# Kernel optimization log

Hardware: AMD Instinct MI355X
Metric: run time of the kernel (lower is better)

## Reference

```python
import jax, jax.numpy as jnp
import numpy as np

B, T, C = 2, 2048, 768
H, N_LEFT = 12, 6
D = C // H


def setup_inputs() -> dict:
    key = jax.random.key(0)
    ks = jax.random.split(key, 4)
    x = jax.random.normal(ks[0], (B, T, C), dtype=jnp.float32)
    attention_mask = jnp.ones((B, T), dtype=jnp.int32)
    Wqkv_w = jax.random.normal(ks[1], (3 * C, C), dtype=jnp.float32) * (C ** -0.5)
    Wqkv_b = jnp.zeros((3 * C,), dtype=jnp.float32)
    Wo_w = jax.random.normal(ks[2], (C, C), dtype=jnp.float32) * (C ** -0.5)
    Wo_b = jnp.zeros((C,), dtype=jnp.float32)
    return {"x": x, "attention_mask": attention_mask, "Wqkv_w": Wqkv_w,
            "Wqkv_b": Wqkv_b, "Wo_w": Wo_w, "Wo_b": Wo_b}


def _attend(q, k, v, mask):
    # q,k,v: [B,h,T,D]; mask: [B,1,T,T] additive
    s = jnp.einsum('bhqd,bhkd->bhqk', q, k) * (D ** -0.5) + mask
    a = jax.nn.softmax(s.astype(jnp.float32), axis=-1).astype(q.dtype)
    return jnp.einsum('bhqk,bhkd->bhqd', a, v)


def reference(x, attention_mask, Wqkv_w, Wqkv_b, Wo_w, Wo_b):
    neg = jnp.finfo(x.dtype).min
    # padding mask [B,1,1,T]: 0 where valid, neg where padded
    pad = (1.0 - attention_mask.astype(x.dtype))[:, None, None, :] * neg
    i = jnp.arange(T)
    tri = (i[None, :] > i[:, None]).astype(x.dtype) * neg   # triu(neg, 1)
    left_mask = tri[None, None] + pad                        # causal (look left)
    right_mask = tri.T[None, None] + pad                     # anti-causal (look right)

    qkv = (x @ Wqkv_w.T + Wqkv_b).reshape(B, T, 3, H, D)
    qkv = jnp.transpose(qkv, (0, 3, 2, 1, 4))                # [B,H,3,T,D]
    q, k, v = qkv[:, :, 0], qkv[:, :, 1], qkv[:, :, 2]

    lc = _attend(q[:, :N_LEFT], k[:, :N_LEFT], v[:, :N_LEFT], left_mask)
    rc = _attend(q[:, N_LEFT:], k[:, N_LEFT:], v[:, N_LEFT:], right_mask)
    ctx = jnp.concatenate([lc, rc], axis=1)                  # [B,H,T,D]
    ctx = jnp.transpose(ctx, (0, 2, 1, 3)).reshape(B, T, C)
    out = ctx @ Wo_w.T + Wo_b
    return out
```

## Files before the change

kernel.cpp:

```cpp
#include <hip/hip_runtime.h>


typedef unsigned short u16;
typedef __bf16 bf16x8 __attribute__((ext_vector_type(8)));
typedef float fx4 __attribute__((ext_vector_type(4)));
typedef unsigned short u16x8 __attribute__((ext_vector_type(8)));
typedef unsigned short u16x4 __attribute__((ext_vector_type(4)));
typedef _Float16 hx4 __attribute__((ext_vector_type(4)));
typedef __fp16 fp16x2 __attribute__((ext_vector_type(2)));

#define T_SEQ 2048
#define C_DIM 768
#define NHEAD 12
#define HDIM  64
#define NITEMS 768
#define LOG2E_8 0.18033688f

__device__ __forceinline__ u16 f2bf(float f) {
  unsigned u = __float_as_uint(f);
  u += 0x7fffu + ((u >> 16) & 1u);
  return (u16)(u >> 16);
}
__device__ __forceinline__ u16 f2h(float f) {
  union { _Float16 h; u16 u; } cv; cv.h = (_Float16)f; return cv.u;
}

__device__ __forceinline__ void gl2lds16(const u16* g, u16* l) {
  __builtin_amdgcn_global_load_lds(
      (const __attribute__((address_space(1))) void*)g,
      (__attribute__((address_space(3))) void*)l, 16, 0, 0);
}

__global__ void cvt_all_k(const float* __restrict__ x,
                          const float* __restrict__ wqkv,
                          const float* __restrict__ wo,
                          const int* __restrict__ am,
                          u16* __restrict__ out, float* __restrict__ mf,
                          unsigned* __restrict__ fbits, int* __restrict__ cnt) {
  if (blockIdx.x >= 2688) {
    int bid = blockIdx.x - 2688;
    int i = bid * blockDim.x + threadIdx.x;
    if (i < 4096) mf[i] = am[i] ? 0.f : -1e30f;
    if (bid == 16) {
      int t = threadIdx.x;
      if (t == 0) cnt[0] = 0;
      if (t < 64) {
        int bb = t >> 5, kt = t & 31;
        const int* seg = am + (bb << 11) + (kt << 6);
        int anyz = 0;
        for (int j = 0; j < 64; ++j) anyz |= (seg[j] == 0);
        unsigned long long bal = __ballot(anyz != 0);
        if (t == 0)  fbits[0] = (unsigned)(bal & 0xffffffffull);
        if (t == 32) fbits[1] = (unsigned)(bal >> 32);
      }
    }
    return;
  }
  int i = blockIdx.x * blockDim.x + threadIdx.x;
  int m = i / 96;
  int c8 = (i - m * 96) << 3;
  const float* src;
  if (m < 4096)       src = x    + (size_t)m * C_DIM + c8;
  else if (m < 6400)  src = wqkv + (size_t)(m - 4096) * C_DIM + c8;
  else                src = wo   + (size_t)(m - 6400) * C_DIM + c8;
  fx4 a = *(const fx4*)src, b = *(const fx4*)(src + 4);
  u16x8 o;
  #pragma unroll
  for (int j = 0; j < 4; ++j) { o[j] = f2bf(a[j]); o[4 + j] = f2bf(b[j]); }
  *(u16x8*)&out[(size_t)m * C_DIM + (c8 ^ ((m & 7) << 3))] = o;
}

__device__ __forceinline__ void gemm_core_64x128(const u16* __restrict__ A,
                                                 const u16* __restrict__ B,
                                                 int m0, int n0,
                                                 u16* As, u16* Bs,
                                                 fx4 acc[4][2]) {
  const int tid = threadIdx.x;
  const int lane = tid & 63, wv = tid >> 6;
  const int wn = wv << 5;
  const int lr = lane & 15, lg = lane >> 4;
  const int swk = (lr & 7) << 3;
  const int scol = (tid & 7) << 3;
  #pragma unroll
  for (int mt = 0; mt < 4; ++mt)
    #pragma unroll
    for (int nt = 0; nt < 2; ++nt) acc[mt][nt] = fx4{0.f, 0.f, 0.f, 0.f};

  #pragma unroll
  for (int p = 0; p < 2; ++p) {
    int row = (tid >> 3) + (p << 5);
    gl2lds16(&A[(size_t)(m0 + row) * C_DIM + scol], &As[(row << 6) + scol]);
  }
  #pragma unroll
  for (int p = 0; p < 4; ++p) {
    int row = (tid >> 3) + (p << 5);
    gl2lds16(&B[(size_t)(n0 + row) * C_DIM + scol], &Bs[(row << 6) + scol]);
  }

  int buf = 0;
  for (int k0 = 0; k0 < C_DIM; k0 += 64, buf ^= 1) {
    __syncthreads();
    if (k0 + 64 < C_DIM) {
      u16* Ad = &As[(buf ^ 1) << 12];
      u16* Bd = &Bs[(buf ^ 1) << 13];
      #pragma unroll
      for (int p = 0; p < 2; ++p) {
        int row = (tid >> 3) + (p << 5);
        gl2lds16(&A[(size_t)(m0 + row) * C_DIM + k0 + 64 + scol], &Ad[(row << 6) + scol]);
      }
      #pragma unroll
      for (int p = 0; p < 4; ++p) {
        int row = (tid >> 3) + (p << 5);
        gl2lds16(&B[(size_t)(n0 + row) * C_DIM + k0 + 64 + scol], &Bd[(row << 6) + scol]);
      }
    }
    const u16* Ab = &As[buf << 12];
    const u16* Bb = &Bs[buf << 13];
    #pragma unroll
    for (int kk = 0; kk < 64; kk += 32) {
      bf16x8 af[4], bfr[2];
      #pragma unroll
      for (int mt = 0; mt < 4; ++mt)
        af[mt] = *(const bf16x8*)&Ab[((mt * 16 + lr) << 6) + ((kk + lg * 8) ^ swk)];
      #pragma unroll
      for (int nt = 0; nt < 2; ++nt)
        bfr[nt] = *(const bf16x8*)&Bb[((wn + nt * 16 + lr) << 6) + ((kk + lg * 8) ^ swk)];
      #pragma unroll
      for (int mt = 0; mt < 4; ++mt)
        #pragma unroll
        for (int nt = 0; nt < 2; ++nt)
          acc[mt][nt] = __builtin_amdgcn_mfma_f32_16x16x32_bf16(
              af[mt], bfr[nt], acc[mt][nt], 0, 0, 0);
    }
  }
}

__global__ __launch_bounds__(256) void gemm_qkv_k(
    const u16* __restrict__ A, const u16* __restrict__ B,
    const float* __restrict__ bias,
    u16* __restrict__ qb, u16* __restrict__ kswz, u16* __restrict__ vswz) {
  __shared__ __align__(16) u16 As[2][64 * 64];
  __shared__ __align__(16) u16 Bs[2][128 * 64];
  int m0 = blockIdx.y << 6, n0 = blockIdx.x << 7;
  fx4 acc[4][2];
  gemm_core_64x128(A, B, m0, n0, &As[0][0], &Bs[0][0], acc);

  const int tid = threadIdx.x, lane = tid & 63, wv = tid >> 6;
  const int wn = wv << 5;
  const int lr = lane & 15, lg = lane >> 4;
  const int part = n0 / 768;
  const int n0r = n0 - part * 768;
  const int bb = m0 >> 11, kt = (m0 >> 6) & 31;
  u16* Sc = &Bs[0][0];
  __syncthreads();

  if (part < 2) {
    #pragma unroll
    for (int nt = 0; nt < 2; ++nt) {
      int nl = wn + nt * 16 + lr;
      float bv = bias[n0 + nl];
      #pragma unroll
      for (int mt = 0; mt < 4; ++mt) {
        #pragma unroll
        for (int r = 0; r < 4; ++r) {
          int m = mt * 16 + lg * 4 + r;
          Sc[(m << 7) + (nl ^ ((m & 15) << 2))] = f2bf(acc[mt][nt][r] + bv);
        }
      }
    }
    __syncthreads();
    int c4 = (tid & 31) << 2;
    int ng = n0r + c4;
    int h = ng >> 6, d = ng & 63;
    int bh = bb * NHEAD + h;
    #pragma unroll
    for (int p = 0; p < 8; ++p) {
      int m = (tid >> 5) + (p << 3);
      u16x4 v = *(const u16x4*)&Sc[(m << 7) + (c4 ^ ((m & 15) << 2))];
      if (part == 0) {
        int t = (m0 & 2047) + m;
        *(u16x4*)&qb[(((size_t)bh << 11) + t) * HDIM + d] = v;
      } else {
        *(u16x4*)&kswz[((size_t)(bh * 32 + kt) << 12) + (m << 6) +
                       (d ^ ((m & 7) << 3))] = v;
      }
    }
  } else {
    #pragma unroll
    for (int nt = 0; nt < 2; ++nt) {
      int nl = wn + nt * 16 + lr;
      float bv = bias[n0 + nl];
      #pragma unroll
      for (int mt = 0; mt < 4; ++mt) {
        u16x4 pk;
        #pragma unroll
        for (int r = 0; r < 4; ++r) pk[r] = f2h(acc[mt][nt][r] + bv);
        int m4 = (mt << 2) + lg;
        *(u16x4*)&Sc[(nl << 6) + ((m4 ^ (nl & 15)) << 2)] = pk;
      }
    }
    __syncthreads();
    int tr4 = tid & 15;
    #pragma unroll
    for (int p = 0; p < 8; ++p) {
      int nl = (tid >> 4) + (p << 4);
      int ng = n0r + nl;
      int h = ng >> 6, d = ng & 63;
      u16x4 v = *(const u16x4*)&Sc[(nl << 6) + ((tr4 ^ (nl & 15)) << 2)];
      size_t tile = (size_t)((bb * NHEAD + h) * 32 + kt) << 12;
      *(u16x4*)&vswz[tile + (d << 6) + ((tr4 ^ (d & 15)) << 2)] = v;
    }
  }
}

__device__ __forceinline__ void gemm_core_64x64(const u16* __restrict__ A,
                                                const u16* __restrict__ B,
                                                int m0, int n0,
                                                u16* As, u16* Bs,
                                                fx4 acc[2][2]) {
  const int tid = threadIdx.x;
  const int lane = tid & 63, wv = tid >> 6;
  const int wm = (wv & 1) << 5, wn = (wv >> 1) << 5;
  const int lr = lane & 15, lg = lane >> 4;
  const int swk = (lr & 7) << 3;
  const int scol = (tid & 7) << 3;
  #pragma unroll
  for (int mt = 0; mt < 2; ++mt)
    #pragma unroll
    for (int nt = 0; nt < 2; ++nt) acc[mt][nt] = fx4{0.f, 0.f, 0.f, 0.f};

  #pragma unroll
  for (int p = 0; p < 2; ++p) {
    int row = (tid >> 3) + (p << 5);
    gl2lds16(&A[(size_t)(m0 + row) * C_DIM + scol], &As[(row << 6) + scol]);
    gl2lds16(&B[(size_t)(n0 + row) * C_DIM + scol], &Bs[(row << 6) + scol]);
  }

  int buf = 0;
  for (int k0 = 0; k0 < C_DIM; k0 += 64, buf ^= 1) {
    __syncthreads();
    if (k0 + 64 < C_DIM) {
      u16* Ad = &As[(buf ^ 1) << 12];
      u16* Bd = &Bs[(buf ^ 1) << 12];
      #pragma unroll
      for (int p = 0; p < 2; ++p) {
        int row = (tid >> 3) + (p << 5);
        gl2lds16(&A[(size_t)(m0 + row) * C_DIM + k0 + 64 + scol], &Ad[(row << 6) + scol]);
        gl2lds16(&B[(size_t)(n0 + row) * C_DIM + k0 + 64 + scol], &Bd[(row << 6) + scol]);
      }
    }
    const u16* Ab = &As[buf << 12];
    const u16* Bb = &Bs[buf << 12];
    #pragma unroll
    for (int kk = 0; kk < 64; kk += 32) {
      bf16x8 af[2], bfr[2];
      #pragma unroll
      for (int mt = 0; mt < 2; ++mt)
        af[mt] = *(const bf16x8*)&Ab[((wm + mt * 16 + lr) << 6) + ((kk + lg * 8) ^ swk)];
      #pragma unroll
      for (int nt = 0; nt < 2; ++nt)
        bfr[nt] = *(const bf16x8*)&Bb[((wn + nt * 16 + lr) << 6) + ((kk + lg * 8) ^ swk)];
      #pragma unroll
      for (int mt = 0; mt < 2; ++mt)
        #pragma unroll
        for (int nt = 0; nt < 2; ++nt)
          acc[mt][nt] = __builtin_amdgcn_mfma_f32_16x16x32_bf16(
              af[mt], bfr[nt], acc[mt][nt], 0, 0, 0);
    }
  }
}

__global__ __launch_bounds__(256) void gemm_out_k(
    const u16* __restrict__ A, const u16* __restrict__ B,
    const float* __restrict__ bias, float* __restrict__ out) {
  __shared__ __align__(16) u16 As[2][64 * 64];
  __shared__ __align__(16) u16 Bs[2][64 * 64];
  int m0 = blockIdx.y << 6, n0 = blockIdx.x << 6;
  fx4 acc[2][2];
  gemm_core_64x64(A, B, m0, n0, &As[0][0], &Bs[0][0], acc);

  const int tid = threadIdx.x, lane = tid & 63, wv = tid >> 6;
  const int wm = (wv & 1) << 5, wn = (wv >> 1) << 5;
  const int lr = lane & 15, lg = lane >> 4;
  #pragma unroll
  for (int nt = 0; nt < 2; ++nt) {
    int n = n0 + wn + nt * 16 + lr;
    float bv = bias[n];
    #pragma unroll
    for (int mt = 0; mt < 2; ++mt) {
      #pragma unroll
      for (int r = 0; r < 4; ++r) {
        int m = m0 + wm + mt * 16 + lg * 4 + r;
        out[(size_t)m * C_DIM + n] = acc[mt][nt][r] + bv;
      }
    }
  }
}

__global__ __launch_bounds__(256) void attn_k(
    const u16* __restrict__ q, const u16* __restrict__ kswz,
    const u16* __restrict__ vswz, const float* __restrict__ maskf,
    const unsigned* __restrict__ fbits,
    u16* __restrict__ ctx, int* __restrict__ counter) {
  __shared__ __align__(16) u16 Ks[2][4096];
  __shared__ __align__(16) u16 Vt[2][4096];
  __shared__ int s_w;

  const int tid = threadIdx.x, lane = tid & 63, wv = tid >> 6;
  const int lr = lane & 15, lg = lane >> 4;
  const int swk = (lr & 7) << 3;
  const int swv = (lr & 15) << 2;

  for (;;) {
    if (tid == 0) s_w = atomicAdd(counter, 1);
    __syncthreads();
    int w = s_w;
    if (w >= NITEMS) break;
    int qslot = w / 24, bh = w - qslot * 24;
    int bb = bh / NHEAD, h = bh - bb * NHEAD;
    bool causal = (h < 6);
    int qt = causal ? (31 - qslot) : qslot;
    int kt0 = causal ? 0 : qt;
    int kt1 = causal ? qt : 31;
    size_t tile_base = (size_t)(bh * 32) << 12;
    unsigned fb = fbits[bb];

    {
      const u16* kg = kswz + tile_base + ((size_t)kt0 << 12);
      const u16* vg = vswz + tile_base + ((size_t)kt0 << 12);
      #pragma unroll
      for (int c2 = 0; c2 < 2; ++c2) {
        int e = (wv << 10) + (c2 << 9) + (lane << 3);
        gl2lds16(kg + e, &Ks[0][e]);
        gl2lds16(vg + e, &Vt[0][e]);
      }
    }

    int q0 = qt << 6;
    size_t head_off = ((size_t)bh << 11) * HDIM;
    int qrow = q0 + wv * 16 + lr;
    bf16x8 qf0 = *(const bf16x8*)&q[head_off + (size_t)qrow * HDIM + lg * 8];
    bf16x8 qf1 = *(const bf16x8*)&q[head_off + (size_t)qrow * HDIM + 32 + lg * 8];
    const float* mrow = maskf + (bb << 11);

    fx4 o[4];
    #pragma unroll
    for (int dt = 0; dt < 4; ++dt) o[dt] = fx4{0.f, 0.f, 0.f, 0.f};
    float l_i = 0.f;

    int buf = 0;
    for (int kt = kt0; kt <= kt1; ++kt, buf ^= 1) {
      __syncthreads();
      if (kt < kt1) {
        const u16* kg = kswz + tile_base + ((size_t)(kt + 1) << 12);
        const u16* vg = vswz + tile_base + ((size_t)(kt + 1) << 12);
        #pragma unroll
        for (int c2 = 0; c2 < 2; ++c2) {
          int e = (wv << 10) + (c2 << 9) + (lane << 3);
          gl2lds16(kg + e, &Ks[buf ^ 1][e]);
          gl2lds16(vg + e, &Vt[buf ^ 1][e]);
        }
      }

      fx4 st[4];
      #pragma unroll
      for (int nt = 0; nt < 4; ++nt) {
        const u16* kr = &Ks[buf][(nt * 16 + lr) << 6];
        bf16x8 kf0 = *(const bf16x8*)&kr[(lg * 8) ^ swk];
        bf16x8 kf1 = *(const bf16x8*)&kr[(32 + lg * 8) ^ swk];
        fx4 z = fx4{0.f, 0.f, 0.f, 0.f};
        z = __builtin_amdgcn_mfma_f32_16x16x32_bf16(kf0, qf0, z, 0, 0, 0);
        st[nt] = __builtin_amdgcn_mfma_f32_16x16x32_bf16(kf1, qf1, z, 0, 0, 0);
      }

      float psum = 0.f;
      if (kt == qt) {
        #pragma unroll
        for (int nt = 0; nt < 4; ++nt) {
          int kb0 = (kt << 6) + nt * 16 + lg * 4;
          fx4 mv = *(const fx4*)&mrow[kb0];
          #pragma unroll
          for (int r = 0; r < 4; ++r) {
            float arg = st[nt][r] * LOG2E_8 + mv[r];
            int kabs = kb0 + r;
            bool dead = causal ? (kabs > qrow) : (kabs < qrow);
            arg = dead ? -1e30f : arg;
            float p = __builtin_amdgcn_exp2f(arg);
            st[nt][r] = p;
            psum += p;
          }
        }
      } else if ((fb >> kt) & 1u) {
        #pragma unroll
        for (int nt = 0; nt < 4; ++nt) {
          int kb0 = (kt << 6) + nt * 16 + lg * 4;
          fx4 mv = *(const fx4*)&mrow[kb0];
          #pragma unroll
          for (int r = 0; r < 4; ++r) {
            float p = __builtin_amdgcn_exp2f(st[nt][r] * LOG2E_8 + mv[r]);
            st[nt][r] = p;
            psum += p;
          }
        }
      } else {
        #pragma unroll
        for (int nt = 0; nt < 4; ++nt)
          #pragma unroll
          for (int r = 0; r < 4; ++r) {
            float p = __builtin_amdgcn_exp2f(st[nt][r] * LOG2E_8);
            st[nt][r] = p;
            psum += p;
          }
      }
      l_i += psum;

      #pragma unroll
      for (int nt = 0; nt < 4; ++nt) {
        union { hx4 v; fp16x2 hh[2]; } pu;
        pu.hh[0] = __builtin_amdgcn_cvt_pkrtz(st[nt][0], st[nt][1]);
        pu.hh[1] = __builtin_amdgcn_cvt_pkrtz(st[nt][2], st[nt][3]);
        hx4 pf = pu.v;
        #pragma unroll
        for (int dt = 0; dt < 4; ++dt) {
          const u16* vr = &Vt[buf][(dt * 16 + lr) << 6];
          hx4 vf = *(const hx4*)&vr[(nt * 16 + lg * 4) ^ swv];
          o[dt] = __builtin_amdgcn_mfma_f32_16x16x16f16(vf, pf, o[dt], 0, 0, 0);
        }
      }
    }

    l_i += __shfl_xor(l_i, 16, 64);
    l_i += __shfl_xor(l_i, 32, 64);
    float inv = 1.f / l_i;
    size_t rowb = ((size_t)(bb << 11) + qrow) * C_DIM;
    int csw = (qrow & 7) << 3;
    #pragma unroll
    for (int dt = 0; dt < 4; ++dt) {
      u16x4 pk;
      #pragma unroll
      for (int r = 0; r < 4; ++r) pk[r] = f2bf(o[dt][r] * inv);
      int colb = h * HDIM + dt * 16 + lg * 4;
      *(u16x4*)&ctx[rowb + (colb ^ csw)] = pk;
    }
  }
}

extern "C" void kernel_launch(void* const* d_in, const int* in_sizes, int n_in,
                              void* d_out, int out_size, void* d_ws, size_t ws_size,
                              hipStream_t stream) {
  const float* x     = (const float*)d_in[0];
  const int*   amask = (const int*)d_in[1];
  const float* wqkv  = (const float*)d_in[2];
  const float* bqkv  = (const float*)d_in[3];
  const float* wo    = (const float*)d_in[4];
  const float* bo    = (const float*)d_in[5];
  float* out = (float*)d_out;

  char* ws = (char*)d_ws;
  u16*      xb    = (u16*)(ws + 0);
  u16*      wqkvb = (u16*)(ws + 6291456);
  u16*      wob   = (u16*)(ws + 9830400);
  u16*      qb    = (u16*)(ws + 11010048);
  u16*      kswz  = (u16*)(ws + 17301504);
  u16*      vswz  = (u16*)(ws + 23592960);
  u16*      ctxb  = (u16*)(ws + 29884416);
  float*    maskf = (float*)(ws + 36175872);
  int*      cnt   = (int*)(ws + 36192256);
  unsigned* fbits = (unsigned*)(ws + 36192320);

  cvt_all_k<<<2705, 256, 0, stream>>>(x, wqkv, wo, amask, xb,
                                      maskf, fbits, cnt);

  gemm_qkv_k<<<dim3(18, 64), 256, 0, stream>>>(xb, wqkvb, bqkv, qb, kswz, vswz);
  attn_k<<<512, 256, 0, stream>>>(qb, kswz, vswz, maskf, fbits, ctxb, cnt);
  gemm_out_k<<<dim3(12, 64), 256, 0, stream>>>(ctxb, wob, bo, out);
}
```

Baseline: 165.7 us.

## Split key tile across waves instead of query rows, reduce partial outputs in LDS

Each wave now takes a 16-key slice of the 64-key tile for all 64 query rows, rather than 16 query rows against all 64 keys. K and V fragments are loaded once per tile per wave and reused across four query groups, which cuts LDS reads, while Q stays in registers as 4x2 fragments. The cost is a cross-wave reduction at the end: partial O accumulators and row sums are combined through LDS with extra barriers. Register pressure also rises because each wave now holds sixteen O accumulators. Softmax keeps using no max subtraction, so the partial sums can simply be added.

Result: faster. 162.4 us (median of 2 runs) (-2.0%).

```diff
diff --git a/kernel.cpp b/kernel.cpp
--- a/kernel.cpp
+++ b/kernel.cpp
@@ -304,12 +304,19 @@
     u16* __restrict__ ctx, int* __restrict__ counter) {
   __shared__ __align__(16) u16 Ks[2][4096];
   __shared__ __align__(16) u16 Vt[2][4096];
+  __shared__ float Ls[4][64];
   __shared__ int s_w;
 
   const int tid = threadIdx.x, lane = tid & 63, wv = tid >> 6;
   const int lr = lane & 15, lg = lane >> 4;
   const int swk = (lr & 7) << 3;
   const int swv = (lr & 15) << 2;
+  const int ke0 = ((wv * 16 + lr) << 6) + ((lg * 8) ^ swk);
+  const int ke1 = ((wv * 16 + lr) << 6) + (((32 + lg * 8)) ^ swk);
+  int vek[4];
+  #pragma unroll
+  for (int dt = 0; dt < 4; ++dt)
+    vek[dt] = ((dt * 16 + lr) << 6) + ((wv * 16 + lg * 4) ^ swv);
 
   for (;;) {
     if (tid == 0) s_w = atomicAdd(counter, 1);
@@ -338,15 +345,21 @@
 
     int q0 = qt << 6;
     size_t head_off = ((size_t)bh << 11) * HDIM;
-    int qrow = q0 + wv * 16 + lr;
-    bf16x8 qf0 = *(const bf16x8*)&q[head_off + (size_t)qrow * HDIM + lg * 8];
-    bf16x8 qf1 = *(const bf16x8*)&q[head_off + (size_t)qrow * HDIM + 32 + lg * 8];
+    bf16x8 qf[4][2];
+    #pragma unroll
+    for (int g = 0; g < 4; ++g) {
+      int qr = q0 + g * 16 + lr;
+      qf[g][0] = *(const bf16x8*)&q[head_off + (size_t)qr * HDIM + lg * 8];
+      qf[g][1] = *(const bf16x8*)&q[head_off + (size_t)qr * HDIM + 32 + lg * 8];
+    }
     const float* mrow = maskf + (bb << 11);
 
-    fx4 o[4];
-    #pragma unroll
-    for (int dt = 0; dt < 4; ++dt) o[dt] = fx4{0.f, 0.f, 0.f, 0.f};
-    float l_i = 0.f;
+    fx4 o[4][4];
+    #pragma unroll
+    for (int dt = 0; dt < 4; ++dt)
+      #pragma unroll
+      for (int g = 0; g < 4; ++g) o[dt][g] = fx4{0.f, 0.f, 0.f, 0.f};
+    float l[4] = {0.f, 0.f, 0.f, 0.f};
 
     int buf = 0;
     for (int kt = kt0; kt <= kt1; ++kt, buf ^= 1) {
@@ -362,85 +375,128 @@
         }
       }
 
+      const u16* kb = &Ks[buf][0];
+      const u16* vbl = &Vt[buf][0];
+
+      bf16x8 kf0 = *(const bf16x8*)&kb[ke0];
+      bf16x8 kf1 = *(const bf16x8*)&kb[ke1];
       fx4 st[4];
       #pragma unroll
-      for (int nt = 0; nt < 4; ++nt) {
-        const u16* kr = &Ks[buf][(nt * 16 + lr) << 6];
-        bf16x8 kf0 = *(const bf16x8*)&kr[(lg * 8) ^ swk];
-        bf16x8 kf1 = *(const bf16x8*)&kr[(32 + lg * 8) ^ swk];
+      for (int g = 0; g < 4; ++g) {
         fx4 z = fx4{0.f, 0.f, 0.f, 0.f};
-        z = __builtin_amdgcn_mfma_f32_16x16x32_bf16(kf0, qf0, z, 0, 0, 0);
-        st[nt] = __builtin_amdgcn_mfma_f32_16x16x32_bf16(kf1, qf1, z, 0, 0, 0);
-      }
-
-      float psum = 0.f;
+        z = __builtin_amdgcn_mfma_f32_16x16x32_bf16(kf0, qf[g][0], z, 0, 0, 0);
+        st[g] = __builtin_amdgcn_mfma_f32_16x16x32_bf16(kf1, qf[g][1], z, 0, 0, 0);
+      }
+
+      int kb0 = (kt << 6) + wv * 16 + lg * 4;
       if (kt == qt) {
-        #pragma unroll
-        for (int nt = 0; nt < 4; ++nt) {
-          int kb0 = (kt << 6) + nt * 16 + lg * 4;
-          fx4 mv = *(const fx4*)&mrow[kb0];
+        fx4 mv = *(const fx4*)&mrow[kb0];
+        #pragma unroll
+        for (int g = 0; g < 4; ++g) {
+          int qr = q0 + g * 16 + lr;
           #pragma unroll
           for (int r = 0; r < 4; ++r) {
-            float arg = st[nt][r] * LOG2E_8 + mv[r];
+            float arg = st[g][r] * LOG2E_8 + mv[r];
             int kabs = kb0 + r;
-            bool dead = causal ? (kabs > qrow) : (kabs < qrow);
+            bool dead = causal ? (kabs > qr) : (kabs < qr);
             arg = dead ? -1e30f : arg;
             float p = __builtin_amdgcn_exp2f(arg);
-            st[nt][r] = p;
-            psum += p;
+            st[g][r] = p;
+            l[g] += p;
           }
         }
       } else if ((fb >> kt) & 1u) {
-        #pragma unroll
-        for (int nt = 0; nt < 4; ++nt) {
-          int kb0 = (kt << 6) + nt * 16 + lg * 4;
-          fx4 mv = *(const fx4*)&mrow[kb0];
+        fx4 mv = *(const fx4*)&mrow[kb0];
+        #pragma unroll
+        for (int g = 0; g < 4; ++g)
           #pragma unroll
           for (int r = 0; r < 4; ++r) {
-            float p = __builtin_amdgcn_exp2f(st[nt][r] * LOG2E_8 + mv[r]);
-            st[nt][r] = p;
-            psum += p;
+            float p = __builtin_amdgcn_exp2f(st[g][r] * LOG2E_8 + mv[r]);
+            st[g][r] = p;
+            l[g] += p;
           }
-        }
       } else {
         #pragma unroll
-        for (int nt = 0; nt < 4; ++nt)
+        for (int g = 0; g < 4; ++g)
           #pragma unroll
           for (int r = 0; r < 4; ++r) {
-            float p = __builtin_amdgcn_exp2f(st[nt][r] * LOG2E_8);
-            st[nt][r] = p;
-            psum += p;
+            float p = __builtin_amdgcn_exp2f(st[g][r] * LOG2E_8);
+            st[g][r] = p;
+            l[g] += p;
           }
       }
-      l_i += psum;
-
-      #pragma unroll
-      for (int nt = 0; nt < 4; ++nt) {
+
+      hx4 pf[4];
+      #pragma unroll
+      for (int g = 0; g < 4; ++g) {
         union { hx4 v; fp16x2 hh[2]; } pu;
-        pu.hh[0] = __builtin_amdgcn_cvt_pkrtz(st[nt][0], st[nt][1]);
-        pu.hh[1] = __builtin_amdgcn_cvt_pkrtz(st[nt][2], st[nt][3]);
-        hx4 pf = pu.v;
-        #pragma unroll
-        for (int dt = 0; dt < 4; ++dt) {
-          const u16* vr = &Vt[buf][(dt * 16 + lr) << 6];
-          hx4 vf = *(const hx4*)&vr[(nt * 16 + lg * 4) ^ swv];
-          o[dt] = __builtin_amdgcn_mfma_f32_16x16x16f16(vf, pf, o[dt], 0, 0, 0);
+        pu.hh[0] = __builtin_amdgcn_cvt_pkrtz(st[g][0], st[g][1]);
+        pu.hh[1] = __builtin_amdgcn_cvt_pkrtz(st[g][2], st[g][3]);
+        pf[g] = pu.v;
+      }
+      #pragma unroll
+      for (int dt = 0; dt < 4; ++dt) {
+        hx4 vf = *(const hx4*)&vbl[vek[dt]];
+        #pragma unroll
+        for (int g = 0; g < 4; ++g)
+          o[dt][g] = __builtin_amdgcn_mfma_f32_16x16x16f16(vf, pf[g], o[dt][g], 0, 0, 0);
+      }
+    }
+
+    __syncthreads();
+    #pragma unroll
+    for (int g = 0; g < 4; ++g) {
+      l[g] += __shfl_xor(l[g], 16, 64);
+      l[g] += __shfl_xor(l[g], 32, 64);
+    }
+    if (lg == 0) {
+      #pragma unroll
+      for (int g = 0; g < 4; ++g) Ls[wv][g * 16 + lr] = l[g];
+    }
+    float* r0 = (float*)&Ks[0][0];
+    float* r1 = (float*)&Vt[0][0];
+    float* rg = (wv & 1) ? r1 : r0;
+    if (wv < 2) {
+      #pragma unroll
+      for (int dt = 0; dt < 4; ++dt)
+        #pragma unroll
+        for (int g = 0; g < 4; ++g) {
+          int qq = g * 16 + lr, c = dt * 4 + lg;
+          *(fx4*)&rg[(qq << 6) + ((c ^ (qq & 15)) << 2)] = o[dt][g];
         }
-      }
-    }
-
-    l_i += __shfl_xor(l_i, 16, 64);
-    l_i += __shfl_xor(l_i, 32, 64);
-    float inv = 1.f / l_i;
-    size_t rowb = ((size_t)(bb << 11) + qrow) * C_DIM;
-    int csw = (qrow & 7) << 3;
-    #pragma unroll
-    for (int dt = 0; dt < 4; ++dt) {
-      u16x4 pk;
-      #pragma unroll
-      for (int r = 0; r < 4; ++r) pk[r] = f2bf(o[dt][r] * inv);
-      int colb = h * HDIM + dt * 16 + lg * 4;
-      *(u16x4*)&ctx[rowb + (colb ^ csw)] = pk;
+    }
+    __syncthreads();
+    if (wv >= 2) {
+      #pragma unroll
+      for (int dt = 0; dt < 4; ++dt)
+        #pragma unroll
+        for (int g = 0; g < 4; ++g) {
+          int qq = g * 16 + lr, c = dt * 4 + lg;
+          float* p = &rg[(qq << 6) + ((c ^ (qq & 15)) << 2)];
+          fx4 cur = *(const fx4*)p;
+          cur += o[dt][g];
+          *(fx4*)p = cur;
+        }
+    }
+    __syncthreads();
+    {
+      int qq = (wv << 4) + lr;
+      float linv = 1.f / (Ls[0][qq] + Ls[1][qq] + Ls[2][qq] + Ls[3][qq]);
+      int tq = q0 + qq;
+      size_t rowb = ((size_t)(bb << 11) + tq) * C_DIM;
+      int csw = (tq & 7) << 3;
+      #pragma unroll
+      for (int j = 0; j < 4; ++j) {
+        int c = (lg << 2) + j;
+        int off = (qq << 6) + ((c ^ (qq & 15)) << 2);
+        fx4 v0 = *(const fx4*)&r0[off];
+        fx4 v1 = *(const fx4*)&r1[off];
+        u16x4 pk;
+        #pragma unroll
+        for (int r = 0; r < 4; ++r) pk[r] = f2bf((v0[r] + v1[r]) * linv);
+        int colb = h * HDIM + (c << 2);
+        *(u16x4*)&ctx[rowb + (colb ^ csw)] = pk;
+      }
     }
   }
 }
```
